# Performance work log

Measured on AMD Instinct MI355X. Metric: run time of the kernel, lower is better.

The kernel has to match this reference:

```python
import jax, jax.numpy as jnp
import numpy as np
from math import log

T, B, IN, H1, H2, OUT = 128, 256, 1024, 2048, 2048, 512
DT, INIT_TAU, MIN_TAU, THRESH, VREST = 0.01, 0.5, 0.1, 1.0, 0.0
SLOPE = 25.0  # snntorch surrogate.fast_sigmoid default slope

@jax.custom_vjp
def spike_fn(x):
    # Heaviside forward; fast-sigmoid surrogate backward
    return (x > 0).astype(x.dtype)

def _spike_fwd(x):
    return spike_fn(x), x

def _spike_bwd(x, g):
    return (g / (SLOPE * jnp.abs(x) + 1.0) ** 2,)

spike_fn.defvjp(_spike_fwd, _spike_bwd)

def setup_inputs() -> dict:
    key = jax.random.key(0)
    ks = jax.random.split(key, 7)
    init_w = -log(1.0 / (INIT_TAU - MIN_TAU) - 1.0)
    def lin(k, fan_in, fan_out):
        bound = 1.0 / np.sqrt(fan_in)
        kw, kb = jax.random.split(k)
        W = jax.random.uniform(kw, (fan_out, fan_in), jnp.float32, -bound, bound)
        b = jax.random.uniform(kb, (fan_out,), jnp.float32, -bound, bound)
        return W, b
    W1, b1 = lin(ks[0], IN, H1)
    W2, b2 = lin(ks[1], H1, H2)
    W3, b3 = lin(ks[2], H2, OUT)
    s = (jax.random.uniform(ks[3], (T, B, IN), jnp.float32) < 0.2).astype(jnp.float32)
    return {
        "s": s,
        "W1": W1, "b1": b1, "wt1": jnp.full((H1,), init_w, jnp.float32),
        "W2": W2, "b2": b2, "wt2": jnp.full((H2,), init_w, jnp.float32),
        "W3": W3, "b3": b3, "wt3": jnp.full((OUT,), init_w, jnp.float32),
    }

def _lif(v, cur, w_tau):
    tau = MIN_TAU + jax.nn.sigmoid(w_tau)
    v = v + (DT / tau) * (-(v - VREST) + cur)  # r = 1.0
    spike = spike_fn(v - THRESH)
    v_post = v * (1.0 - spike)  # zero reset
    return v_post, spike, v  # v is pre-reset membrane (v_tmp)

def reference(s, W1, b1, wt1, W2, b2, wt2, W3, b3, wt3):
    v0 = (jnp.zeros((B, H1), s.dtype), jnp.zeros((B, H2), s.dtype), jnp.zeros((B, OUT), s.dtype))
    def step(carry, st):
        v1, v2, v3 = carry
        v1, s1, _ = _lif(v1, st @ W1.T + b1, wt1)
        v2, s2, _ = _lif(v2, s1 @ W2.T + b2, wt2)
        v3, s3, vtmp = _lif(v3, s2 @ W3.T + b3, wt3)
        return (v1, v2, v3), (s3, vtmp)
    _, (out_s, out_v) = jax.lax.scan(step, v0, s)
    return out_s, out_v
```

## Files before the change

kernel.cpp:

```cpp
#include <hip/hip_runtime.h>
#include <hip/hip_bf16.h>
#include <cstdint>
#include <cstddef>

#define T_STEPS 128
#define BATCH   256
#define IN_F    1024
#define H1_F    2048
#define H2_F    2048
#define OUT_F   512
#define M_TOT   (T_STEPS * BATCH)

#define W1_SCALE 4064.0f
#define W1_INV   (1.0f / 4064.0f)

#define S_F4_BLOCKS 8192
#define W_F4_BLOCKS 512

typedef __attribute__((ext_vector_type(4))) int   int4v;
typedef __attribute__((ext_vector_type(8))) unsigned short ushort8;
typedef unsigned long long ull;

__device__ __forceinline__ void load16_to_lds(const void* g, void* l) {
  __builtin_amdgcn_global_load_lds(
      (const __attribute__((address_space(1))) void*)g,
      (__attribute__((address_space(3))) void*)l, 16, 0, 0);
}

__device__ __forceinline__ unsigned short f2bf(float x) {
  __hip_bfloat16 h = __float2bfloat16(x);
  return *reinterpret_cast<unsigned short*>(&h);
}

__device__ __forceinline__ float bf2f(unsigned short u) {
  unsigned int w = ((unsigned int)u) << 16;
  return *reinterpret_cast<float*>(&w);
}

__device__ __forceinline__ float lif_k(float w) {
  float tau = 0.1f + 1.0f / (1.0f + expf(-w));
  return 0.01f / tau;
}

__global__ __launch_bounds__(256) void cvt_both(
    const float4* __restrict__ s_in, unsigned int* __restrict__ s_out,
    const float4* __restrict__ w_in, unsigned int* __restrict__ w_out) {
  const int tid = threadIdx.x, lane = tid & 63, wv = tid >> 6;
  const int bid = blockIdx.x;
  const bool is_s = bid < S_F4_BLOCKS;
  const float4* in;
  unsigned int* out;
  size_t base;
  if (is_s) {
    in = s_in; out = s_out;
    base = (size_t)bid * 1024 + wv * 256 + lane;
  } else {
    in = w_in; out = w_out;
    base = (size_t)(bid - S_F4_BLOCKS) * 1024 + wv * 256 + lane;
  }
#pragma unroll
  for (int q = 0; q < 4; ++q) {
    float4 v = in[base + q * 64];
    unsigned int p;
    if (is_s) {
      p = (v.x > 0.5f ? 1u : 0u) | (v.y > 0.5f ? 0x100u : 0u) |
          (v.z > 0.5f ? 0x10000u : 0u) | (v.w > 0.5f ? 0x1000000u : 0u);
    } else {
      int c0 = __float2int_rn(v.x * W1_SCALE), c1 = __float2int_rn(v.y * W1_SCALE);
      int c2 = __float2int_rn(v.z * W1_SCALE), c3 = __float2int_rn(v.w * W1_SCALE);
      p = (c0 & 0xff) | ((c1 & 0xff) << 8) | ((c2 & 0xff) << 16) | ((c3 & 0xff) << 24);
    }
    out[base + q * 64] = p;
  }
}

union SMem {
  struct { uint4 lA[1024]; uint4 lB[1024]; } st;
  unsigned short tile[128 * 136];
};

__global__ __launch_bounds__(256) void gemm_scan(
    const int8_t* __restrict__ A, const int8_t* __restrict__ B,
    const float* __restrict__ b1, const float* __restrict__ wt1,
    ull* __restrict__ mask1) {
  __shared__ SMem sm;
  const int K = IN_F;
  const int tid = threadIdx.x, lane = tid & 63, wv = tid >> 6;
  const int wm = (wv & 1) * 64, wn = (wv >> 1) * 64;

  const int id = blockIdx.x;
  const int xcd = id & 7, j = id >> 3;
  const int bblk = xcd * 32 + (j >> 4);
  const int n0   = (j & 15) * 128;

  const int mk = lane & 15, grp = lane >> 4;

  int4v acc[4][4] = {};

  for (int kt = 0; kt < K; kt += 128) {
#pragma unroll
    for (int i = 0; i < 4; ++i) {
      int cellbase = (wv * 4 + i) * 64;
      int cell = cellbase + lane;
      int r  = cell >> 3;
      int kb = (cell & 7) ^ (r & 7);
      load16_to_lds(A + (size_t)(r * BATCH + bblk) * K + kt + kb * 16, &sm.st.lA[cellbase]);
      load16_to_lds(B + (size_t)(n0 + r) * K + kt + kb * 16, &sm.st.lB[cellbase]);
    }
    __syncthreads();
#pragma unroll
    for (int ks = 0; ks < 2; ++ks) {
      int4v af[4], bfr[4];
      const int kb = ks * 4 + grp;
#pragma unroll
      for (int f = 0; f < 4; ++f) {
        int m = wm + f * 16 + mk;
        af[f]  = *(const int4v*)&sm.st.lA[m * 8 + (kb ^ (m & 7))];
        int n = wn + f * 16 + mk;
        bfr[f] = *(const int4v*)&sm.st.lB[n * 8 + (kb ^ (n & 7))];
      }
#pragma unroll
      for (int i = 0; i < 4; ++i)
#pragma unroll
        for (int jj = 0; jj < 4; ++jj)
          acc[i][jj] = __builtin_amdgcn_mfma_i32_16x16x64_i8(af[i], bfr[jj], acc[i][jj], 0, 0, 0);
    }
    __syncthreads();
  }

#pragma unroll
  for (int jj = 0; jj < 4; ++jj) {
    const int h = wn + jj * 16 + mk;
#pragma unroll
    for (int i = 0; i < 4; ++i) {
      const int t0 = wm + i * 16 + grp * 4;
      uint2 pk;
      pk.x = ((unsigned int)f2bf((float)acc[i][jj][1] * W1_INV) << 16)
           | f2bf((float)acc[i][jj][0] * W1_INV);
      pk.y = ((unsigned int)f2bf((float)acc[i][jj][3] * W1_INV) << 16)
           | f2bf((float)acc[i][jj][2] * W1_INV);
      *(uint2*)&sm.tile[h * 136 + t0] = pk;
    }
  }
  __syncthreads();

  if (tid < 128) {
    const int h  = tid;
    const int hg = n0 + h;
    const int wv2 = tid >> 6;
    const int ln  = tid & 63;
    const float bias = b1[hg];
    const float k    = lif_k(wt1[hg]);
    const size_t wbase = (size_t)(n0 >> 6) + wv2;
    float v = 0.0f;
    for (int t8 = 0; t8 < T_STEPS; t8 += 8) {
      ushort8 pk = *(const ushort8*)&sm.tile[h * 136 + t8];
#pragma unroll
      for (int u = 0; u < 8; ++u) {
        v = fmaf(k, (bf2f(pk[u]) + bias) - v, v);
        bool sp = v > 1.0f;
        ull bm = __ballot(sp);
        if (ln == 0)
          mask1[((size_t)(t8 + u) * BATCH + bblk) * (H1_F / 64) + wbase] = bm;
        if (sp) v = 0.0f;
      }
    }
  }
}

__global__ __launch_bounds__(1024) void layer23_kernel(
    const ull* __restrict__ mask1,
    const float* __restrict__ W2, const float* __restrict__ b2, const float* __restrict__ wt2,
    const float* __restrict__ W3, const float* __restrict__ b3, const float* __restrict__ wt3,
    float* __restrict__ out_s, float* __restrict__ out_v) {
  __shared__ ull m1all[T_STEPS * 32];
  __shared__ ull m2sh[2][32];
  const int tid = threadIdx.x, b = blockIdx.x;
  const int lane = tid & 63, wv = tid >> 6;

  const float bias2a = b2[tid], bias2b = b2[tid + 1024];
  const float k2a = lif_k(wt2[tid]), k2b = lif_k(wt2[tid + 1024]);
  const float* W2a = W2 + (size_t)tid * H1_F;
  const float* W2b = W2 + (size_t)(tid + 1024) * H1_F;
  float v2a = 0.0f, v2b = 0.0f;

  float bias3 = 0.0f, k3 = 0.0f, v3 = 0.0f;
  const float* W3r = W3;
  if (wv < 8) {
    bias3 = b3[tid];
    k3 = lif_k(wt3[tid]);
    W3r = W3 + (size_t)tid * H2_F;
  }

#pragma unroll
  for (int u = 0; u < 4; ++u) {
    int idx = tid + u * 1024;
    m1all[idx] = mask1[((size_t)(idx >> 5) * BATCH + b) * 32 + (idx & 31)];
  }
  __syncthreads();

  for (int t = 0; t < T_STEPS; ++t) {
    ull wrd = (lane < 32) ? m1all[t * 32 + lane] : 0ull;

    float cura = bias2a, curb = bias2b;
    if (__ballot(wrd != 0ull)) {
      for (int wi = 0; wi < 32; ++wi) {
        ull m = __shfl(wrd, wi, 64);
        while (m) {
          int bit = __ffsll(m) - 1;
          m &= m - 1;
          int idx = wi * 64 + bit;
          cura += W2a[idx];
          curb += W2b[idx];
        }
      }
    }
    v2a = fmaf(k2a, cura - v2a, v2a);
    v2b = fmaf(k2b, curb - v2b, v2b);
    bool spa = v2a > 1.0f, spb = v2b > 1.0f;
    ull sa = __ballot(spa);
    ull sb = __ballot(spb);
    if (lane == 0) { m2sh[t & 1][wv] = sa; m2sh[t & 1][16 + wv] = sb; }
    if (spa) v2a = 0.0f;
    if (spb) v2b = 0.0f;
    __syncthreads();

    if (wv < 8) {
      ull w3m = (lane < 32) ? m2sh[t & 1][lane] : 0ull;
      float cur3 = bias3;
      if (__ballot(w3m != 0ull)) {
        for (int wi = 0; wi < 32; ++wi) {
          ull m = __shfl(w3m, wi, 64);
          while (m) {
            int bit = __ffsll(m) - 1;
            m &= m - 1;
            cur3 += W3r[wi * 64 + bit];
          }
        }
      }
      float vp = fmaf(k3, cur3 - v3, v3);
      bool sp = vp > 1.0f;
      size_t idx = (size_t)(t * BATCH + b) * OUT_F + tid;
      out_s[idx] = sp ? 1.0f : 0.0f;
      out_v[idx] = vp;
      v3 = sp ? 0.0f : vp;
    }
  }
}

extern "C" void kernel_launch(void* const* d_in, const int* in_sizes, int n_in,
                              void* d_out, int out_size, void* d_ws, size_t ws_size,
                              hipStream_t stream) {
  const float* s   = (const float*)d_in[0];
  const float* W1  = (const float*)d_in[1];
  const float* b1  = (const float*)d_in[2];
  const float* wt1 = (const float*)d_in[3];
  const float* W2  = (const float*)d_in[4];
  const float* b2  = (const float*)d_in[5];
  const float* wt2 = (const float*)d_in[6];
  const float* W3  = (const float*)d_in[7];
  const float* b3  = (const float*)d_in[8];
  const float* wt3 = (const float*)d_in[9];

  char* wsb = (char*)d_ws;
  const size_t MASK_BYTES = (size_t)T_STEPS * BATCH * (H1_F / 64) * 8;
  const size_t S_ELEMS  = (size_t)M_TOT * IN_F;
  ull* mask1 = (ull*)wsb;
  int8_t* s_i8  = (int8_t*)(wsb + MASK_BYTES);
  int8_t* W1_i8 = s_i8 + S_ELEMS;
  (void)ws_size;

  float* outs = (float*)d_out;
  float* outv = outs + (size_t)T_STEPS * BATCH * OUT_F;

  cvt_both<<<S_F4_BLOCKS + W_F4_BLOCKS, 256, 0, stream>>>(
      (const float4*)s, (unsigned int*)s_i8, (const float4*)W1, (unsigned int*)W1_i8);

  gemm_scan<<<BATCH * (H1_F / 128), 256, 0, stream>>>(s_i8, W1_i8, b1, wt1, mask1);

  layer23_kernel<<<BATCH, 1024, 0, stream>>>(mask1, W2, b2, wt2, W3, b3, wt3, outs, outv);
}
```

Before: 379.3 us.

## Enlarge gemm_scan tiles to 256x256 with double-buffered LDS and 8 waves

The layer-1 int8 GEMM+scan kernel now uses 512-thread blocks computing 256x256 tiles (two batch elements by 256 hidden units), with double-buffered async global-to-LDS staging and explicit vmcnt waits so loads overlap MFMA work. Per-phase barriers and s_setprio are added to interleave waves, and the scan now uses all 8 waves, covering two batch elements. This aims to raise operand reuse and hide load latency. In exchange it raises LDS use (~128KB per block via the union) and register pressure from 32 accumulators, and the many extra barriers may cost occupancy.

```diff
diff --git a/kernel.cpp b/kernel.cpp
--- a/kernel.cpp
+++ b/kernel.cpp
@@ -75,93 +75,120 @@
 }
 
 union SMem {
-  struct { uint4 lA[1024]; uint4 lB[1024]; } st;
-  unsigned short tile[128 * 136];
+  struct { uint4 lA[2][2048]; uint4 lB[2][2048]; } st;
+  unsigned short tile[2][256][136];
 };
 
-__global__ __launch_bounds__(256) void gemm_scan(
+__device__ __forceinline__ void stage_tiles(
+    const int8_t* __restrict__ A, const int8_t* __restrict__ B,
+    uint4* lA, uint4* lB, int tid, int b0, int n0, int kt) {
+#pragma unroll
+  for (int u = 0; u < 4; ++u) {
+    const int s = tid + u * 512;
+    const int r = s >> 3;
+    const int csw = ((s & 7) ^ (r & 7)) * 16;
+    load16_to_lds(A + (size_t)((r & 127) * BATCH + b0 + (r >> 7)) * IN_F + kt + csw,
+                  &lA[s]);
+    load16_to_lds(B + (size_t)(n0 + r) * IN_F + kt + csw, &lB[s]);
+  }
+}
+
+__global__ __launch_bounds__(512, 2) void gemm_scan(
     const int8_t* __restrict__ A, const int8_t* __restrict__ B,
     const float* __restrict__ b1, const float* __restrict__ wt1,
     ull* __restrict__ mask1) {
   __shared__ SMem sm;
-  const int K = IN_F;
   const int tid = threadIdx.x, lane = tid & 63, wv = tid >> 6;
-  const int wm = (wv & 1) * 64, wn = (wv >> 1) * 64;
+  const int mk = lane & 15, grp = lane >> 4;
+  const int wr = wv >> 2, wc = wv & 3;
 
   const int id = blockIdx.x;
-  const int xcd = id & 7, j = id >> 3;
-  const int bblk = xcd * 32 + (j >> 4);
-  const int n0   = (j & 15) * 128;
-
-  const int mk = lane & 15, grp = lane >> 4;
-
-  int4v acc[4][4] = {};
-
-  for (int kt = 0; kt < K; kt += 128) {
-#pragma unroll
-    for (int i = 0; i < 4; ++i) {
-      int cellbase = (wv * 4 + i) * 64;
-      int cell = cellbase + lane;
-      int r  = cell >> 3;
-      int kb = (cell & 7) ^ (r & 7);
-      load16_to_lds(A + (size_t)(r * BATCH + bblk) * K + kt + kb * 16, &sm.st.lA[cellbase]);
-      load16_to_lds(B + (size_t)(n0 + r) * K + kt + kb * 16, &sm.st.lB[cellbase]);
-    }
-    __syncthreads();
-#pragma unroll
-    for (int ks = 0; ks < 2; ++ks) {
-      int4v af[4], bfr[4];
-      const int kb = ks * 4 + grp;
+  const int nt = id & 7, mt = id >> 3;
+  const int b0 = mt * 2;
+  const int n0 = nt * 256;
+
+  int4v acc[8][4] = {};
+
+  stage_tiles(A, B, sm.st.lA[0], sm.st.lB[0], tid, b0, n0, 0);
+
+  for (int t = 0; t < 8; ++t) {
+    const int cur = t & 1;
+    if (t < 7) {
+      stage_tiles(A, B, sm.st.lA[cur ^ 1], sm.st.lB[cur ^ 1], tid, b0, n0, (t + 1) * 128);
+      asm volatile("s_waitcnt vmcnt(8)" ::: "memory");
+    } else {
+      asm volatile("s_waitcnt vmcnt(0)" ::: "memory");
+    }
+    __builtin_amdgcn_sched_barrier(0);
+    __builtin_amdgcn_s_barrier();
+    __builtin_amdgcn_sched_barrier(0);
+
+#pragma unroll
+    for (int p = 0; p < 8; ++p) {
+      const int ks = p >> 2, mh = (p >> 1) & 1, nh = p & 1;
+      int4v af[4], bfr[2];
 #pragma unroll
       for (int f = 0; f < 4; ++f) {
-        int m = wm + f * 16 + mk;
-        af[f]  = *(const int4v*)&sm.st.lA[m * 8 + (kb ^ (m & 7))];
-        int n = wn + f * 16 + mk;
-        bfr[f] = *(const int4v*)&sm.st.lB[n * 8 + (kb ^ (n & 7))];
-      }
+        const int m = wr * 128 + (mh * 4 + f) * 16 + mk;
+        af[f] = *(const int4v*)&sm.st.lA[cur][m * 8 + ((ks * 4 + grp) ^ (m & 7))];
+      }
+#pragma unroll
+      for (int f = 0; f < 2; ++f) {
+        const int n = wc * 64 + (nh * 2 + f) * 16 + mk;
+        bfr[f] = *(const int4v*)&sm.st.lB[cur][n * 8 + ((ks * 4 + grp) ^ (n & 7))];
+      }
+      __builtin_amdgcn_sched_barrier(0);
+      __builtin_amdgcn_s_barrier();
+      __builtin_amdgcn_sched_barrier(0);
+      __builtin_amdgcn_s_setprio(1);
 #pragma unroll
       for (int i = 0; i < 4; ++i)
 #pragma unroll
-        for (int jj = 0; jj < 4; ++jj)
-          acc[i][jj] = __builtin_amdgcn_mfma_i32_16x16x64_i8(af[i], bfr[jj], acc[i][jj], 0, 0, 0);
-    }
-    __syncthreads();
-  }
-
-#pragma unroll
-  for (int jj = 0; jj < 4; ++jj) {
-    const int h = wn + jj * 16 + mk;
-#pragma unroll
-    for (int i = 0; i < 4; ++i) {
-      const int t0 = wm + i * 16 + grp * 4;
+        for (int j = 0; j < 2; ++j)
+          acc[mh * 4 + i][nh * 2 + j] = __builtin_amdgcn_mfma_i32_16x16x64_i8(
+              af[i], bfr[j], acc[mh * 4 + i][nh * 2 + j], 0, 0, 0);
+      __builtin_amdgcn_s_setprio(0);
+      __builtin_amdgcn_sched_barrier(0);
+      __builtin_amdgcn_s_barrier();
+      __builtin_amdgcn_sched_barrier(0);
+    }
+  }
+
+#pragma unroll
+  for (int j = 0; j < 4; ++j) {
+    const int h = wc * 64 + j * 16 + mk;
+#pragma unroll
+    for (int i = 0; i < 8; ++i) {
+      const int t0 = i * 16 + grp * 4;
       uint2 pk;
-      pk.x = ((unsigned int)f2bf((float)acc[i][jj][1] * W1_INV) << 16)
-           | f2bf((float)acc[i][jj][0] * W1_INV);
-      pk.y = ((unsigned int)f2bf((float)acc[i][jj][3] * W1_INV) << 16)
-           | f2bf((float)acc[i][jj][2] * W1_INV);
-      *(uint2*)&sm.tile[h * 136 + t0] = pk;
+      pk.x = ((unsigned int)f2bf((float)acc[i][j][1] * W1_INV) << 16)
+           | f2bf((float)acc[i][j][0] * W1_INV);
+      pk.y = ((unsigned int)f2bf((float)acc[i][j][3] * W1_INV) << 16)
+           | f2bf((float)acc[i][j][2] * W1_INV);
+      *(uint2*)&sm.tile[wr][h][t0] = pk;
     }
   }
   __syncthreads();
 
-  if (tid < 128) {
-    const int h  = tid;
+  {
+    const int bl = wv >> 2;
+    const int hw = wv & 3;
+    const int h  = hw * 64 + lane;
     const int hg = n0 + h;
-    const int wv2 = tid >> 6;
-    const int ln  = tid & 63;
+    const int b  = b0 + bl;
     const float bias = b1[hg];
     const float k    = lif_k(wt1[hg]);
-    const size_t wbase = (size_t)(n0 >> 6) + wv2;
+    const size_t wbase = (size_t)(n0 >> 6) + hw;
     float v = 0.0f;
     for (int t8 = 0; t8 < T_STEPS; t8 += 8) {
-      ushort8 pk = *(const ushort8*)&sm.tile[h * 136 + t8];
+      ushort8 pk = *(const ushort8*)&sm.tile[bl][h][t8];
 #pragma unroll
       for (int u = 0; u < 8; ++u) {
         v = fmaf(k, (bf2f(pk[u]) + bias) - v, v);
         bool sp = v > 1.0f;
         ull bm = __ballot(sp);
-        if (ln == 0)
-          mask1[((size_t)(t8 + u) * BATCH + bblk) * (H1_F / 64) + wbase] = bm;
+        if (lane == 0)
+          mask1[((size_t)(t8 + u) * BATCH + b) * (H1_F / 64) + wbase] = bm;
         if (sp) v = 0.0f;
       }
     }
@@ -276,7 +303,7 @@
   cvt_both<<<S_F4_BLOCKS + W_F4_BLOCKS, 256, 0, stream>>>(
       (const float4*)s, (unsigned int*)s_i8, (const float4*)W1, (unsigned int*)W1_i8);
 
-  gemm_scan<<<BATCH * (H1_F / 128), 256, 0, stream>>>(s_i8, W1_i8, b1, wt1, mask1);
+  gemm_scan<<<(BATCH / 2) * (H1_F / 256), 512, 0, stream>>>(s_i8, W1_i8, b1, wt1, mask1);
 
   layer23_kernel<<<BATCH, 1024, 0, stream>>>(mask1, W2, b2, wt2, W3, b3, wt3, outs, outv);
 }
```

New measurement: 397.8 us. 4.9% more time.
